# Kernel optimization log

Measured on AMD Instinct MI355X. Metric: run time of the kernel, lower is better.

## Reference

```python
import jax, jax.numpy as jnp
import numpy as np

HIDDEN = 768
HEADS = 12
ORDERS = 3
NEG = -1e9


def setup_inputs() -> dict:
    key = jax.random.key(0)
    ks = jax.random.split(key, 16)
    B, N = 8, 512
    s = 0.02
    inp = {
        "v": jax.random.normal(ks[0], (B, N, HIDDEN), jnp.float32),
        "k": jax.random.normal(ks[1], (B, N, HIDDEN), jnp.float32),
        "q": jax.random.normal(ks[2], (B, N, HIDDEN), jnp.float32),
        "masks": jax.random.bernoulli(ks[3], 0.1, (ORDERS, B, 1, N, N)),
        "tau": 1,
        "training": 0,
        "Wv": jax.random.normal(ks[4], (HIDDEN, HIDDEN), jnp.float32) * s,
        "bv": jnp.zeros((HIDDEN,), jnp.float32),
        "Wk": jax.random.normal(ks[5], (HIDDEN, HIDDEN), jnp.float32) * s,
        "bk": jnp.zeros((HIDDEN,), jnp.float32),
        "Wq": jax.random.normal(ks[6], (HIDDEN, HIDDEN), jnp.float32) * s,
        "bq": jnp.zeros((HIDDEN,), jnp.float32),
        "Wm": jax.random.normal(ks[7], (HIDDEN, HIDDEN), jnp.float32) * s,
        "bm": jnp.zeros((HIDDEN,), jnp.float32),
        "pool_w": jax.random.normal(ks[8], (HIDDEN, 1), jnp.float32) * s,
        "pool_b": jnp.zeros((1,), jnp.float32),
        "mlp_w1": jax.random.normal(ks[9], (HIDDEN, HIDDEN // 2), jnp.float32) * s,
        "mlp_w2": jax.random.normal(ks[10], (HIDDEN // 2, ORDERS), jnp.float32) * s,
        "mlp_b2": jnp.zeros((ORDERS,), jnp.float32),
    }
    return inp


def _soft_routing(x, pool_w, pool_b, mlp_w1, mlp_w2, mlp_b2):
    # pooling='fc': masked attention pooling over sequence, then 2-layer MLP + softmax
    pad = (jnp.sum(jnp.abs(x), axis=-1) == 0)[:, :, None]        # [B, N, 1]
    scores = x @ pool_w + pool_b                                  # [B, N, 1]
    scores = jnp.where(pad, NEG, scores)
    scores = jax.nn.softmax(scores, axis=1)
    pooled = jnp.sum(x * scores, axis=1)                          # [B, HIDDEN]
    logits = jax.nn.relu(pooled @ mlp_w1) @ mlp_w2 + mlp_b2       # [B, L]
    return jax.nn.softmax(logits, axis=-1)


def reference(v, k, q, masks, tau, training, Wv, bv, Wk, bk, Wq, bq, Wm, bm,
              pool_w, pool_b, mlp_w1, mlp_w2, mlp_b2):
    B, N, _ = q.shape
    dk = HIDDEN // HEADS
    alphas = _soft_routing(v, pool_w, pool_b, mlp_w1, mlp_w2, mlp_b2)  # [B, L]

    def split_heads(x):
        return x.reshape(B, N, HEADS, dk).transpose(0, 2, 1, 3)  # [B, H, N, dk]

    vh = split_heads(v @ Wv + bv)
    kh = split_heads(k @ Wk + bk)
    qh = split_heads(q @ Wq + bq)

    scores = jnp.einsum('bhnd,bhmd->bhnm', qh, kh) / jnp.sqrt(jnp.float32(dk))
    # masks: [L, B, 1, N, N] broadcast over heads -> att_list [L, B, H, N, N]
    masked = jnp.where(masks[:, :, :, :, :], NEG, scores[None])
    att_list = jax.nn.softmax(masked, axis=-1)                    # [L, B, H, N, N]
    att_map = jnp.einsum('bl,lbhnm->bhnm', alphas, att_list)
    atted = jnp.einsum('bhnm,bhmd->bhnd', att_map, vh)
    atted = atted.transpose(0, 2, 1, 3).reshape(B, N, HIDDEN)
    return atted @ Wm + bm
```

## Files before the change

### kernel.cpp

```cpp
#include <hip/hip_runtime.h>
#include <hip/hip_bf16.h>
#include <stdint.h>


typedef __bf16 bf16x8 __attribute__((ext_vector_type(8)));
typedef float f32x4 __attribute__((ext_vector_type(4)));

#define NEGV -1e9f

__device__ __forceinline__ float b2f(unsigned short h) {
    union { unsigned int u; float f; } x; x.u = ((unsigned int)h) << 16; return x.f;
}
__device__ __forceinline__ unsigned short f2b(float f) {
    union { float f; unsigned int u; } x; x.f = f;
    unsigned int u = x.u + 0x7FFFu + ((x.u >> 16) & 1u);
    return (unsigned short)(u >> 16);
}
__device__ __forceinline__ unsigned int packbf(unsigned int u0, unsigned int u1) {
    unsigned int r0 = (u0 + 0x7FFFu + ((u0 >> 16) & 1u)) >> 16;
    unsigned int r1 = (u1 + 0x7FFFu + ((u1 >> 16) & 1u)) & 0xFFFF0000u;
    return r0 | r1;
}
__device__ __forceinline__ uint4 load8bf(const void* base, size_t elemOff, int isF32) {
    if (!isF32) return *(const uint4*)((const unsigned short*)base + elemOff);
    const uint4* f = (const uint4*)((const float*)base + elemOff);
    uint4 a = f[0], b = f[1];
    uint4 r;
    r.x = packbf(a.x, a.y);
    r.y = packbf(a.z, a.w);
    r.z = packbf(b.x, b.y);
    r.w = packbf(b.z, b.w);
    return r;
}
__device__ __forceinline__ float loadF(const void* p, int idx, int isF32) {
    return isF32 ? ((const float*)p)[idx] : b2f(((const unsigned short*)p)[idx]);
}

__global__ void sniff_kernel(const unsigned int* __restrict__ mp,
                             const unsigned int* __restrict__ vp,
                             const unsigned int* __restrict__ wp,
                             int* __restrict__ flags)
{
    __shared__ int oki, oku, okf, badv, badw;
    if (threadIdx.x == 0) { oki = 1; oku = 1; okf = 1; badv = 0; badw = 0; }
    __syncthreads();
    int li = 1, lu = 1, lf = 1, bv = 0, bw = 0;
    for (int i = threadIdx.x; i < 16384; i += 256) {
        unsigned int w = mp[i];
        if (w > 1u) li = 0;
        if (w & 0xFEFEFEFEu) lu = 0;
        if (w != 0u && w != 0x3F800000u) lf = 0;
    }
    for (int i = threadIdx.x; i < 8192; i += 256) {
        unsigned int w = vp[i];
        float f0 = b2f((unsigned short)(w & 0xFFFF));
        float f1 = b2f((unsigned short)(w >> 16));
        if (!(fabsf(f0) < 1e4f) || !(fabsf(f1) < 1e4f)) bv = 1;
        w = wp[i];
        f0 = b2f((unsigned short)(w & 0xFFFF));
        f1 = b2f((unsigned short)(w >> 16));
        if (!(fabsf(f0) < 1e4f) || !(fabsf(f1) < 1e4f)) bw = 1;
    }
    if (!li) atomicAnd(&oki, 0);
    if (!lu) atomicAnd(&oku, 0);
    if (!lf) atomicAnd(&okf, 0);
    if (bv) atomicOr(&badv, 1);
    if (bw) atomicOr(&badw, 1);
    __syncthreads();
    if (threadIdx.x == 0) {
        flags[0] = oki ? 0 : (oku ? 1 : (okf ? 2 : 3));
        flags[1] = badv;
        flags[2] = badw;
    }
}

__global__ __launch_bounds__(256) void conv_act_kernel(
        const void* __restrict__ v, const void* __restrict__ k,
        const void* __restrict__ q, const int* __restrict__ flags,
        unsigned short* __restrict__ vb, unsigned short* __restrict__ kb,
        unsigned short* __restrict__ qb)
{
    const int dtV = flags[1];
    const int which = blockIdx.y;
    const void* src = (which == 0) ? v : (which == 1) ? k : q;
    unsigned short* dst = (which == 0) ? vb : (which == 1) ? kb : qb;
    size_t off = ((size_t)blockIdx.x * 256 + threadIdx.x) * 8;
    uint4 r = load8bf(src, off, dtV);
    *(uint4*)(dst + off) = r;
}

__global__ __launch_bounds__(256) void conv_wt_kernel(
        const void* __restrict__ W0, const void* __restrict__ W1,
        const void* __restrict__ W2, const void* __restrict__ W3,
        const int* __restrict__ flags,
        unsigned short* __restrict__ T0, unsigned short* __restrict__ T1,
        unsigned short* __restrict__ T2, unsigned short* __restrict__ T3)
{
    __shared__ unsigned short tile[64][65];
    const int t = threadIdx.x;
    const int dtW = flags[2];
    const int which = blockIdx.y;
    const void* W = (which == 0) ? W0 : (which == 1) ? W1 : (which == 2) ? W2 : W3;
    unsigned short* T = (which == 0) ? T0 : (which == 1) ? T1 : (which == 2) ? T2 : T3;
    const int tk = (blockIdx.x / 12) << 6;
    const int tn = (blockIdx.x % 12) << 6;
    #pragma unroll
    for (int i = 0; i < 16; i++) {
        int idx = (i << 8) + t;
        int r = idx >> 6, c = idx & 63;
        tile[r][c] = f2b(loadF(W, (tk + r) * 768 + tn + c, dtW));
    }
    __syncthreads();
    #pragma unroll
    for (int i = 0; i < 16; i++) {
        int idx = (i << 8) + t;
        int rn = idx >> 6, ck = idx & 63;
        T[(size_t)(tn + rn) * 768 + tk + ck] = tile[ck][rn];
    }
}

__global__ __launch_bounds__(256) void pack_kernel(
        const void* __restrict__ masks, const int* __restrict__ flags,
        unsigned int* __restrict__ pm)
{
    __shared__ unsigned char flg[32 * 512];
    const int t = threadIdx.x;
    const int mode = flags[0];
    const size_t e0 = (size_t)blockIdx.x * (32 * 512);
    if (mode == 0 || mode == 2) {
        const uint4* p = (const uint4*)((const unsigned int*)masks + e0);
        for (int i = t; i < 4096; i += 256) {
            uint4 u = p[i];
            int base = i << 2;
            flg[base + 0] = u.x ? 1 : 0;
            flg[base + 1] = u.y ? 1 : 0;
            flg[base + 2] = u.z ? 1 : 0;
            flg[base + 3] = u.w ? 1 : 0;
        }
    } else if (mode == 1) {
        const uint4* p = (const uint4*)((const unsigned char*)masks + e0);
        for (int i = t; i < 1024; i += 256) {
            uint4 u = p[i];
            unsigned int uu[4] = {u.x, u.y, u.z, u.w};
            int base = i << 4;
            #pragma unroll
            for (int k2 = 0; k2 < 4; k2++)
                #pragma unroll
                for (int bb = 0; bb < 4; bb++)
                    flg[base + k2 * 4 + bb] = ((uu[k2] >> (bb * 8)) & 0xFFu) ? 1 : 0;
        }
    } else {
        const uint4* p = (const uint4*)((const unsigned short*)masks + e0);
        for (int i = t; i < 2048; i += 256) {
            uint4 u = p[i];
            unsigned int uu[4] = {u.x, u.y, u.z, u.w};
            int base = i << 3;
            #pragma unroll
            for (int k2 = 0; k2 < 4; k2++) {
                flg[base + k2 * 2 + 0] = (uu[k2] & 0xFFFFu) ? 1 : 0;
                flg[base + k2 * 2 + 1] = (uu[k2] >> 16) ? 1 : 0;
            }
        }
    }
    __syncthreads();
    for (int widx = t; widx < 512; widx += 256) {
        int rl = widx >> 4, lm = widx & 15;
        unsigned int bits = 0;
        #pragma unroll
        for (int g = 0; g < 32; g++)
            bits |= ((unsigned int)(flg[rl * 512 + (g << 4) + lm] & 1)) << g;
        pm[(size_t)blockIdx.x * 512 + widx] = bits;
    }
}

__global__ __launch_bounds__(256) void route_score_kernel(
        const void* __restrict__ v, const void* __restrict__ pool_w,
        const void* __restrict__ pool_b, const int* __restrict__ flags,
        float* __restrict__ scores)
{
    __shared__ float pw[768];
    const int t = threadIdx.x;
    const int b = blockIdx.x >> 3, ch = blockIdx.x & 7;
    const int dtV = flags[1], dtW = flags[2];
    for (int d = t; d < 768; d += 256) pw[d] = loadF(pool_w, d, dtW);
    __syncthreads();
    const int r = t >> 2, c4 = t & 3;
    const int n = (ch << 6) + r;
    float dot = 0.f, asum = 0.f;
    if (!dtV) {
        const unsigned int* vr = (const unsigned int*)v + ((size_t)(b * 512 + n)) * 384;
        for (int j = 0; j < 96; j++) {
            int p = c4 + (j << 2);
            unsigned int u = vr[p];
            float f0 = b2f((unsigned short)(u & 0xFFFF));
            float f1 = b2f((unsigned short)(u >> 16));
            asum += fabsf(f0) + fabsf(f1);
            dot += f0 * pw[2 * p] + f1 * pw[2 * p + 1];
        }
    } else {
        const float* vf = (const float*)v + ((size_t)(b * 512 + n)) * 768;
        for (int j = 0; j < 48; j++) {
            float4 u = ((const float4*)vf)[c4 + (j << 2)];
            int e = (c4 + (j << 2)) << 2;
            asum += fabsf(u.x) + fabsf(u.y) + fabsf(u.z) + fabsf(u.w);
            dot += u.x * pw[e] + u.y * pw[e + 1] + u.z * pw[e + 2] + u.w * pw[e + 3];
        }
    }
    dot += __shfl_xor(dot, 1); dot += __shfl_xor(dot, 2);
    asum += __shfl_xor(asum, 1); asum += __shfl_xor(asum, 2);
    if (c4 == 0)
        scores[b * 512 + n] = (asum == 0.f) ? NEGV : dot + loadF(pool_b, 0, dtW);
}

__global__ __launch_bounds__(512) void route_softmax_kernel(
        const float* __restrict__ scores, float* __restrict__ scs)
{
    __shared__ float red[8];
    const int t = threadIdx.x, b = blockIdx.x;
    float scv = scores[b * 512 + t];
    float mx = scv;
    #pragma unroll
    for (int off = 1; off < 64; off <<= 1) mx = fmaxf(mx, __shfl_xor(mx, off));
    if ((t & 63) == 0) red[t >> 6] = mx;
    __syncthreads();
    float M = red[0];
    #pragma unroll
    for (int i = 1; i < 8; i++) M = fmaxf(M, red[i]);
    float e = __expf(scv - M);
    __syncthreads();
    float sm = e;
    #pragma unroll
    for (int off = 1; off < 64; off <<= 1) sm += __shfl_xor(sm, off);
    if ((t & 63) == 0) red[t >> 6] = sm;
    __syncthreads();
    float SS = 0.f;
    #pragma unroll
    for (int i = 0; i < 8; i++) SS += red[i];
    scs[b * 512 + t] = e / SS;
}

__global__ __launch_bounds__(256) void route_pool_kernel(
        const void* __restrict__ v, const int* __restrict__ flags,
        const float* __restrict__ scs, float* __restrict__ ppart)
{
    __shared__ float ps[64];
    const int t = threadIdx.x;
    const int ch = blockIdx.x, b = blockIdx.y;
    const int dtV = flags[1];
    if (t < 64) ps[t] = scs[b * 512 + (ch << 6) + t];
    __syncthreads();
    const int d0 = t * 3;
    float a0 = 0.f, a1 = 0.f, a2 = 0.f;
    if (!dtV) {
        const unsigned short* vb = (const unsigned short*)v
            + ((size_t)(b * 512 + (ch << 6))) * 768 + d0;
        #pragma unroll 4
        for (int r = 0; r < 64; r++) {
            float p = ps[r];
            a0 += b2f(vb[0]) * p; a1 += b2f(vb[1]) * p; a2 += b2f(vb[2]) * p;
            vb += 768;
        }
    } else {
        const float* vb = (const float*)v + ((size_t)(b * 512 + (ch << 6))) * 768 + d0;
        #pragma unroll 4
        for (int r = 0; r < 64; r++) {
            float p = ps[r];
            a0 += vb[0] * p; a1 += vb[1] * p; a2 += vb[2] * p;
            vb += 768;
        }
    }
    float* o = ppart + ((size_t)(b * 8 + ch)) * 768 + d0;
    o[0] = a0; o[1] = a1; o[2] = a2;
}

__global__ __launch_bounds__(256) void route_hid_kernel(
        const void* __restrict__ w1, const void* __restrict__ w2,
        const int* __restrict__ flags, const float* __restrict__ ppart,
        float* __restrict__ plog)
{
    __shared__ float pool[768];
    __shared__ float red[4][32];
    const int t = threadIdx.x;
    const int jc = blockIdx.x, b = blockIdx.y;
    const int dtW = flags[2];
    for (int d = t; d < 768; d += 256) {
        float a = 0.f;
        #pragma unroll
        for (int c = 0; c < 8; c++) a += ppart[((size_t)(b * 8 + c)) * 768 + d];
        pool[d] = a;
    }
    __syncthreads();
    const int jo = (t & 3) << 3;
    const int dr = t >> 2;
    float acc[8];
    #pragma unroll
    for (int j = 0; j < 8; j++) acc[j] = 0.f;
    for (int it = 0; it < 12; it++) {
        int d = (it << 6) + dr;
        float pv = pool[d];
        size_t off = (size_t)d * 384 + (jc << 5) + jo;
        if (!dtW) {
            uint4 u = *(const uint4*)((const unsigned short*)w1 + off);
            unsigned int uu[4] = {u.x, u.y, u.z, u.w};
            #pragma unroll
            for (int j2 = 0; j2 < 4; j2++) {
                acc[2 * j2]     += pv * b2f((unsigned short)(uu[j2] & 0xFFFF));
                acc[2 * j2 + 1] += pv * b2f((unsigned short)(uu[j2] >> 16));
            }
        } else {
            const float4* f = (const float4*)((const float*)w1 + off);
            float4 u0 = f[0], u1 = f[1];
            acc[0] += pv * u0.x; acc[1] += pv * u0.y;
            acc[2] += pv * u0.z; acc[3] += pv * u0.w;
            acc[4] += pv * u1.x; acc[5] += pv * u1.y;
            acc[6] += pv * u1.z; acc[7] += pv * u1.w;
        }
    }
    #pragma unroll
    for (int off = 4; off < 64; off <<= 1)
        #pragma unroll
        for (int j = 0; j < 8; j++) acc[j] += __shfl_xor(acc[j], off);
    const int w = t >> 6, lane = t & 63;
    if (lane < 4) {
        #pragma unroll
        for (int j = 0; j < 8; j++) red[w][lane * 8 + j] = acc[j];
    }
    __syncthreads();
    if (t < 32) {
        float h = red[0][t] + red[1][t] + red[2][t] + red[3][t];
        h = fmaxf(h, 0.f);
        int jg = (jc << 5) + t;
        float l0 = h * loadF(w2, jg * 3 + 0, dtW);
        float l1 = h * loadF(w2, jg * 3 + 1, dtW);
        float l2 = h * loadF(w2, jg * 3 + 2, dtW);
        #pragma unroll
        for (int off = 1; off < 32; off <<= 1) {
            l0 += __shfl_xor(l0, off);
            l1 += __shfl_xor(l1, off);
            l2 += __shfl_xor(l2, off);
        }
        if (t == 0) {
            float* o = plog + ((size_t)(b * 12 + jc)) * 3;
            o[0] = l0; o[1] = l1; o[2] = l2;
        }
    }
}

__global__ __launch_bounds__(64) void route_alpha_kernel(
        const void* __restrict__ b2, const int* __restrict__ flags,
        const float* __restrict__ plog, float* __restrict__ alphas)
{
    const int t = threadIdx.x, b = blockIdx.x;
    if (t == 0) {
        const int dtW = flags[2];
        float lg[3];
        #pragma unroll
        for (int l = 0; l < 3; l++) {
            float a = loadF(b2, l, dtW);
            for (int jc = 0; jc < 12; jc++) a += plog[((size_t)(b * 12 + jc)) * 3 + l];
            lg[l] = a;
        }
        float mm = fmaxf(lg[0], fmaxf(lg[1], lg[2]));
        float e0 = __expf(lg[0] - mm), e1 = __expf(lg[1] - mm), e2 = __expf(lg[2] - mm);
        float ss = e0 + e1 + e2;
        alphas[b * 3 + 0] = e0 / ss;
        alphas[b * 3 + 1] = e1 / ss;
        alphas[b * 3 + 2] = e2 / ss;
    }
}

__global__ __launch_bounds__(256) void gemm_kernel(
        const unsigned short* __restrict__ X,
        const unsigned short* __restrict__ WT,
        const void* __restrict__ bias,
        const int* __restrict__ flags,
        void* __restrict__ dst, int mode)
{
    __shared__ unsigned short smem[64 * 72];
    unsigned short* At = smem;
    unsigned short* Bt = smem + 2048;
    const int t = threadIdx.x;
    const int id = blockIdx.x;
    const int bx = id >> 6, by = id & 63;
    const int w = t >> 6, lane = t & 63, q = lane >> 4, lm = lane & 15;
    const int row0 = by << 6, col0 = bx << 6;
    const int ar = t >> 2, ac = (t & 3) << 3;
    const int aswz = ((ar >> 3) & 3) << 3;
    const int am = (w << 4) + lm;
    const int acs = ((am >> 3) & 3) << 3;
    const int dtW = flags[2];
    const int dtOut = flags[1];

    f32x4 acc[4];
    #pragma unroll
    for (int i = 0; i < 4; i++) acc[i] = (f32x4){0.f, 0.f, 0.f, 0.f};

    const unsigned short* xp = X + (size_t)(row0 + ar) * 768 + ac;
    const unsigned short* wp = WT + (size_t)(col0 + ar) * 768 + ac;
    for (int k0 = 0; k0 < 768; k0 += 32) {
        uint4 av = *(const uint4*)(xp + k0);
        uint4 wv = *(const uint4*)(wp + k0);
        __syncthreads();
        *(uint4*)(&At[ar * 32 + (ac ^ aswz)]) = av;
        *(uint4*)(&Bt[ar * 32 + (ac ^ aswz)]) = wv;
        __syncthreads();
        bf16x8 afr = *(const bf16x8*)(&At[am * 32 + ((q << 3) ^ acs)]);
        #pragma unroll
        for (int t4 = 0; t4 < 4; t4++) {
            int bn = (t4 << 4) + lm;
            bf16x8 bfr = *(const bf16x8*)(&Bt[bn * 32 + ((q << 3) ^ (((bn >> 3) & 3) << 3))]);
            acc[t4] = __builtin_amdgcn_mfma_f32_16x16x32_bf16(afr, bfr, acc[t4], 0, 0, 0);
        }
    }

    if (mode == 1 && dtOut) {
        #pragma unroll
        for (int t4 = 0; t4 < 4; t4++) {
            int col = col0 + (t4 << 4) + lm;
            float bsv = loadF(bias, col, dtW);
            #pragma unroll
            for (int rg = 0; rg < 4; rg++) {
                int row = row0 + (w << 4) + (q << 2) + rg;
                ((float*)dst)[(size_t)row * 768 + col] = acc[t4][rg] + bsv;
            }
        }
        return;
    }

    __syncthreads();
    #pragma unroll
    for (int t4 = 0; t4 < 4; t4++) {
        int colL = (t4 << 4) + lm;
        float bsv = loadF(bias, col0 + colL, dtW);
        #pragma unroll
        for (int rg = 0; rg < 4; rg++) {
            int rowL = (w << 4) + (q << 2) + rg;
            unsigned short hv = f2b(acc[t4][rg] + bsv);
            if (mode == 2) smem[colL * 72 + rowL] = hv;
            else           smem[rowL * 72 + colL] = hv;
        }
    }
    __syncthreads();
    const int g = t >> 2, c0 = (t & 3) << 4;
    uint4 w0 = *(const uint4*)&smem[g * 72 + c0];
    uint4 w1v = *(const uint4*)&smem[g * 72 + c0 + 8];
    unsigned short* o;
    if (mode == 0) {
        int b = row0 >> 9, n0b = row0 & 511, h = col0 >> 6;
        o = (unsigned short*)dst + ((size_t)(b * 12 + h) * 512 + n0b + g) * 64 + c0;
    } else if (mode == 2) {
        int b = row0 >> 9, n0b = row0 & 511, h = col0 >> 6;
        o = (unsigned short*)dst + ((size_t)(b * 12 + h) * 64 + g) * 512 + n0b + c0;
    } else {
        o = (unsigned short*)dst + (size_t)(row0 + g) * 768 + col0 + c0;
    }
    *(uint4*)o = w0;
    *(uint4*)(o + 8) = w1v;
}

__global__ __launch_bounds__(256) void attn_kernel(
        const unsigned short* __restrict__ qh, const unsigned short* __restrict__ kh,
        const unsigned short* __restrict__ vT, const unsigned int* __restrict__ pm,
        const float* __restrict__ alphas, unsigned short* __restrict__ atted)
{
    __shared__ unsigned short P[16 * 512];
    __shared__ float Zp[4][16][3];
    __shared__ unsigned short Ost[16 * 72];
    const int t = threadIdx.x;
    const int w = t >> 6, lane = t & 63, quad = lane >> 4, lm = lane & 15;
    const int id = blockIdx.x;
    const int bh = id % 96, qb = id / 96;
    const int b = bh / 12, h = bh % 12;
    const int n0 = qb << 4;

    const unsigned short* qrow = qh + ((size_t)(bh * 512 + n0 + lm)) * 64 + (quad << 3);
    bf16x8 qa0 = *(const bf16x8*)qrow;
    bf16x8 qa1 = *(const bf16x8*)(qrow + 32);
    f32x4 acc[8];
    #pragma unroll
    for (int i = 0; i < 8; i++) acc[i] = (f32x4){0.f, 0.f, 0.f, 0.f};
    const unsigned short* kb0 = kh + ((size_t)(bh * 512 + (w << 7) + lm)) * 64 + (quad << 3);
    #pragma unroll
    for (int nt = 0; nt < 8; nt++) {
        const unsigned short* kr = kb0 + nt * (16 * 64);
        bf16x8 k0 = *(const bf16x8*)kr;
        bf16x8 k1 = *(const bf16x8*)(kr + 32);
        acc[nt] = __builtin_amdgcn_mfma_f32_16x16x32_bf16(qa0, k0, acc[nt], 0, 0, 0);
        acc[nt] = __builtin_amdgcn_mfma_f32_16x16x32_bf16(qa1, k1, acc[nt], 0, 0, 0);
    }

    float al[3];
    #pragma unroll
    for (int l = 0; l < 3; l++) al[l] = alphas[b * 3 + l];

    #pragma unroll
    for (int nt = 0; nt < 8; nt++)
        #pragma unroll
        for (int rg = 0; rg < 4; rg++)
            acc[nt][rg] = __expf(acc[nt][rg] * 0.125f);

    unsigned int mk[4][3];
    #pragma unroll
    for (int rg = 0; rg < 4; rg++)
        #pragma unroll
        for (int l = 0; l < 3; l++)
            mk[rg][l] = pm[((size_t)((l << 3) + b) * 512 + n0 + (quad << 2) + rg) * 16 + lm];

    #pragma unroll
    for (int rg = 0; rg < 4; rg++) {
        float z0 = 0.f, z1 = 0.f, z2 = 0.f;
        #pragma unroll
        for (int nt = 0; nt < 8; nt++) {
            int g = (w << 3) + nt;
            float e = acc[nt][rg];
            if (!((mk[rg][0] >> g) & 1)) z0 += e;
            if (!((mk[rg][1] >> g) & 1)) z1 += e;
            if (!((mk[rg][2] >> g) & 1)) z2 += e;
        }
        #pragma unroll
        for (int off = 1; off < 16; off <<= 1) {
            z0 += __shfl_xor(z0, off);
            z1 += __shfl_xor(z1, off);
            z2 += __shfl_xor(z2, off);
        }
        if (lm == 0) {
            int row = (quad << 2) + rg;
            Zp[w][row][0] = z0; Zp[w][row][1] = z1; Zp[w][row][2] = z2;
        }
    }
    __syncthreads();

    #pragma unroll
    for (int rg = 0; rg < 4; rg++) {
        int row = (quad << 2) + rg;
        float coef[3]; float addu = 0.f;
        #pragma unroll
        for (int l = 0; l < 3; l++) {
            float Z = Zp[0][row][l] + Zp[1][row][l] + Zp[2][row][l] + Zp[3][row][l];
            if (Z > 0.f) coef[l] = al[l] / Z;
            else { coef[l] = 0.f; addu += al[l] * (1.0f / 512.0f); }
        }
        #pragma unroll
        for (int nt = 0; nt < 8; nt++) {
            int g = (w << 3) + nt;
            float p = addu;
            float e = acc[nt][rg];
            if (!((mk[rg][0] >> g) & 1)) p += coef[0] * e;
            if (!((mk[rg][1] >> g) & 1)) p += coef[1] * e;
            if (!((mk[rg][2] >> g) & 1)) p += coef[2] * e;
            int c = (g << 4) + lm;
            int chunk = c >> 3, j = c & 7;
            P[row * 512 + (((chunk ^ (row & 7))) << 3) + j] = f2b(p);
        }
    }
    __syncthreads();

    f32x4 accO = (f32x4){0.f, 0.f, 0.f, 0.f};
    const unsigned short* vb = vT + ((size_t)(bh * 64 + (w << 4) + lm)) * 512 + (quad << 3);
    #pragma unroll
    for (int ks = 0; ks < 16; ks++) {
        bf16x8 pa = *(const bf16x8*)&P[lm * 512 + ((((ks << 2) + quad) ^ (lm & 7)) << 3)];
        bf16x8 vf = *(const bf16x8*)(vb + (ks << 5));
        accO = __builtin_amdgcn_mfma_f32_16x16x32_bf16(pa, vf, accO, 0, 0, 0);
    }
    #pragma unroll
    for (int rg = 0; rg < 4; rg++)
        Ost[((quad << 2) + rg) * 72 + (w << 4) + lm] = f2b(accO[rg]);
    __syncthreads();
    const int r2 = t >> 4, c4 = t & 15;
    uint2 val = *(const uint2*)&Ost[r2 * 72 + (c4 << 2)];
    *(uint2*)&atted[((size_t)(b * 512 + n0 + r2)) * 768 + (h << 6) + (c4 << 2)] = val;
}

extern "C" void kernel_launch(void* const* d_in, const int* in_sizes, int n_in,
                              void* d_out, int out_size, void* d_ws, size_t ws_size,
                              hipStream_t stream)
{
    const void* v  = d_in[0];
    const void* k  = d_in[1];
    const void* q  = d_in[2];
    const void* mk = d_in[3];
    const void* Wv = d_in[6];
    const void* bv = d_in[7];
    const void* Wk = d_in[8];
    const void* bk = d_in[9];
    const void* Wq = d_in[10];
    const void* bq = d_in[11];
    const void* Wm = d_in[12];
    const void* bm = d_in[13];
    const void* pool_w = d_in[14];
    const void* pool_b = d_in[15];
    const void* w1 = d_in[16];
    const void* w2 = d_in[17];
    const void* b2 = d_in[18];

    char* ws = (char*)d_ws;
    int*   flags  = (int*)ws;
    float* alphas = (float*)(ws + 256);
    float* scores = (float*)(ws + 512);
    float* scs    = (float*)(ws + 16896);
    float* ppart  = (float*)(ws + 33280);
    float* plog   = (float*)(ws + 229888);
    unsigned int* pm = (unsigned int*)(ws + 262144);
    unsigned short* qh  = (unsigned short*)(ws + 1048576);
    unsigned short* kh  = (unsigned short*)(ws + 1048576 + 1 * 6291456L);
    unsigned short* vT  = (unsigned short*)(ws + 1048576 + 2 * 6291456L);
    unsigned short* vb  = (unsigned short*)(ws + 1048576 + 3 * 6291456L);
    unsigned short* kb  = (unsigned short*)(ws + 1048576 + 4 * 6291456L);
    unsigned short* qb  = (unsigned short*)(ws + 1048576 + 5 * 6291456L);
    unsigned short* atted = vb;
    char* wt0 = ws + 1048576 + 6 * 6291456L;
    unsigned short* WTv = (unsigned short*)(wt0);
    unsigned short* WTk = (unsigned short*)(wt0 + 1 * 1179648L);
    unsigned short* WTq = (unsigned short*)(wt0 + 2 * 1179648L);
    unsigned short* WTm = (unsigned short*)(wt0 + 3 * 1179648L);

    sniff_kernel<<<dim3(1), dim3(256), 0, stream>>>(
        (const unsigned int*)mk, (const unsigned int*)v, (const unsigned int*)Wv, flags);
    conv_act_kernel<<<dim3(1536, 3), dim3(256), 0, stream>>>(v, k, q, flags, vb, kb, qb);
    conv_wt_kernel<<<dim3(144, 4), dim3(256), 0, stream>>>(
        Wv, Wk, Wq, Wm, flags, WTv, WTk, WTq, WTm);
    pack_kernel<<<dim3(384), dim3(256), 0, stream>>>(mk, flags, pm);
    route_score_kernel<<<dim3(64), dim3(256), 0, stream>>>(v, pool_w, pool_b, flags, scores);
    route_softmax_kernel<<<dim3(8), dim3(512), 0, stream>>>(scores, scs);
    route_pool_kernel<<<dim3(8, 8), dim3(256), 0, stream>>>(v, flags, scs, ppart);
    route_hid_kernel<<<dim3(12, 8), dim3(256), 0, stream>>>(w1, w2, flags, ppart, plog);
    route_alpha_kernel<<<dim3(8), dim3(64), 0, stream>>>(b2, flags, plog, alphas);
    gemm_kernel<<<dim3(768), dim3(256), 0, stream>>>(vb, WTv, bv, flags, (void*)vT, 2);
    gemm_kernel<<<dim3(768), dim3(256), 0, stream>>>(kb, WTk, bk, flags, (void*)kh, 0);
    gemm_kernel<<<dim3(768), dim3(256), 0, stream>>>(qb, WTq, bq, flags, (void*)qh, 0);
    attn_kernel<<<dim3(3072), dim3(256), 0, stream>>>(qh, kh, vT, pm, alphas, atted);
    gemm_kernel<<<dim3(768), dim3(256), 0, stream>>>(atted, WTm, bm, flags, d_out, 1);
}
```

Measured before the change: 314.0 us.

## Batch QKV projections into one launch and prefetch deeper K tiles in GEMM

The three Q/K/V projection GEMMs become a single launch that selects its operands by blockIdx.y, which cuts launch count and fills the GPU with more concurrent blocks. The GEMM K-step grows from 32 to 64 with an XOR-swizzled shared layout, and global loads for the next tile are issued before the MFMAs on the current tile, halving barriers and overlapping load latency. The attention kernel pre-shifts its mask words per wave to simplify the bit tests. Doubling shared memory per block may reduce occupancy.

```diff
diff --git a/kernel.cpp b/kernel.cpp
--- a/kernel.cpp
+++ b/kernel.cpp
@@ -369,48 +369,74 @@
     }
 }
 
-__global__ __launch_bounds__(256) void gemm_kernel(
-        const unsigned short* __restrict__ X,
-        const unsigned short* __restrict__ WT,
-        const void* __restrict__ bias,
+__global__ __launch_bounds__(256) void gemm3_kernel(
+        const unsigned short* __restrict__ X0, const unsigned short* __restrict__ X1,
+        const unsigned short* __restrict__ X2,
+        const unsigned short* __restrict__ W0, const unsigned short* __restrict__ W1,
+        const unsigned short* __restrict__ W2,
+        const void* __restrict__ bias0, const void* __restrict__ bias1,
+        const void* __restrict__ bias2,
         const int* __restrict__ flags,
-        void* __restrict__ dst, int mode)
-{
-    __shared__ unsigned short smem[64 * 72];
+        void* __restrict__ dst0, void* __restrict__ dst1, void* __restrict__ dst2,
+        int m0, int m1, int m2)
+{
+    __shared__ unsigned short smem[8192];
     unsigned short* At = smem;
-    unsigned short* Bt = smem + 2048;
+    unsigned short* Bt = smem + 4096;
     const int t = threadIdx.x;
+    const int which = blockIdx.y;
+    const unsigned short* X  = (which == 0) ? X0 : (which == 1) ? X1 : X2;
+    const unsigned short* WT = (which == 0) ? W0 : (which == 1) ? W1 : W2;
+    const void* bias = (which == 0) ? bias0 : (which == 1) ? bias1 : bias2;
+    void* dst = (which == 0) ? dst0 : (which == 1) ? dst1 : dst2;
+    const int mode = (which == 0) ? m0 : (which == 1) ? m1 : m2;
+
     const int id = blockIdx.x;
     const int bx = id >> 6, by = id & 63;
-    const int w = t >> 6, lane = t & 63, q = lane >> 4, lm = lane & 15;
     const int row0 = by << 6, col0 = bx << 6;
-    const int ar = t >> 2, ac = (t & 3) << 3;
-    const int aswz = ((ar >> 3) & 3) << 3;
-    const int am = (w << 4) + lm;
-    const int acs = ((am >> 3) & 3) << 3;
+    const int w = t >> 6, lane = t & 63, quad = lane >> 4, lm = lane & 15;
+    const int r0 = t >> 3, c0 = (t & 7) << 3;
+    const int wr0 = r0 * 64 + (c0 ^ ((r0 & 7) << 3));
     const int dtW = flags[2];
     const int dtOut = flags[1];
 
+    const unsigned short* xp  = X  + (size_t)(row0 + r0) * 768 + c0;
+    const unsigned short* xp2 = xp + 32 * 768;
+    const unsigned short* wp  = WT + (size_t)(col0 + r0) * 768 + c0;
+    const unsigned short* wp2 = wp + 32 * 768;
+
+    uint4 a0 = *(const uint4*)xp,  a1 = *(const uint4*)xp2;
+    uint4 g0 = *(const uint4*)wp,  g1 = *(const uint4*)wp2;
+
     f32x4 acc[4];
     #pragma unroll
     for (int i = 0; i < 4; i++) acc[i] = (f32x4){0.f, 0.f, 0.f, 0.f};
 
-    const unsigned short* xp = X + (size_t)(row0 + ar) * 768 + ac;
-    const unsigned short* wp = WT + (size_t)(col0 + ar) * 768 + ac;
-    for (int k0 = 0; k0 < 768; k0 += 32) {
-        uint4 av = *(const uint4*)(xp + k0);
-        uint4 wv = *(const uint4*)(wp + k0);
+    const int am = (w << 4) + lm;
+    const int abase = am * 64, akey = (am & 7) << 3;
+
+    for (int k0 = 0;;) {
         __syncthreads();
-        *(uint4*)(&At[ar * 32 + (ac ^ aswz)]) = av;
-        *(uint4*)(&Bt[ar * 32 + (ac ^ aswz)]) = wv;
+        *(uint4*)&At[wr0] = a0;        *(uint4*)&At[wr0 + 2048] = a1;
+        *(uint4*)&Bt[wr0] = g0;        *(uint4*)&Bt[wr0 + 2048] = g1;
         __syncthreads();
-        bf16x8 afr = *(const bf16x8*)(&At[am * 32 + ((q << 3) ^ acs)]);
-        #pragma unroll
-        for (int t4 = 0; t4 < 4; t4++) {
-            int bn = (t4 << 4) + lm;
-            bf16x8 bfr = *(const bf16x8*)(&Bt[bn * 32 + ((q << 3) ^ (((bn >> 3) & 3) << 3))]);
-            acc[t4] = __builtin_amdgcn_mfma_f32_16x16x32_bf16(afr, bfr, acc[t4], 0, 0, 0);
-        }
+        k0 += 64;
+        if (k0 < 768) {
+            a0 = *(const uint4*)(xp + k0);  a1 = *(const uint4*)(xp2 + k0);
+            g0 = *(const uint4*)(wp + k0);  g1 = *(const uint4*)(wp2 + k0);
+        }
+        #pragma unroll
+        for (int ks = 0; ks < 2; ks++) {
+            int ko = (quad << 3) + (ks << 5);
+            bf16x8 afr = *(const bf16x8*)&At[abase + (ko ^ akey)];
+            #pragma unroll
+            for (int t4 = 0; t4 < 4; t4++) {
+                int bn = (t4 << 4) + lm;
+                bf16x8 bfr = *(const bf16x8*)&Bt[bn * 64 + (ko ^ ((bn & 7) << 3))];
+                acc[t4] = __builtin_amdgcn_mfma_f32_16x16x32_bf16(afr, bfr, acc[t4], 0, 0, 0);
+            }
+        }
+        if (k0 >= 768) break;
     }
 
     if (mode == 1 && dtOut) {
@@ -420,7 +446,7 @@
             float bsv = loadF(bias, col, dtW);
             #pragma unroll
             for (int rg = 0; rg < 4; rg++) {
-                int row = row0 + (w << 4) + (q << 2) + rg;
+                int row = row0 + (w << 4) + (quad << 2) + rg;
                 ((float*)dst)[(size_t)row * 768 + col] = acc[t4][rg] + bsv;
             }
         }
@@ -434,28 +460,28 @@
         float bsv = loadF(bias, col0 + colL, dtW);
         #pragma unroll
         for (int rg = 0; rg < 4; rg++) {
-            int rowL = (w << 4) + (q << 2) + rg;
+            int rowL = (w << 4) + (quad << 2) + rg;
             unsigned short hv = f2b(acc[t4][rg] + bsv);
             if (mode == 2) smem[colL * 72 + rowL] = hv;
             else           smem[rowL * 72 + colL] = hv;
         }
     }
     __syncthreads();
-    const int g = t >> 2, c0 = (t & 3) << 4;
-    uint4 w0 = *(const uint4*)&smem[g * 72 + c0];
-    uint4 w1v = *(const uint4*)&smem[g * 72 + c0 + 8];
+    const int g = t >> 2, cc = (t & 3) << 4;
+    uint4 o0 = *(const uint4*)&smem[g * 72 + cc];
+    uint4 o1 = *(const uint4*)&smem[g * 72 + cc + 8];
     unsigned short* o;
     if (mode == 0) {
         int b = row0 >> 9, n0b = row0 & 511, h = col0 >> 6;
-        o = (unsigned short*)dst + ((size_t)(b * 12 + h) * 512 + n0b + g) * 64 + c0;
+        o = (unsigned short*)dst + ((size_t)(b * 12 + h) * 512 + n0b + g) * 64 + cc;
     } else if (mode == 2) {
         int b = row0 >> 9, n0b = row0 & 511, h = col0 >> 6;
-        o = (unsigned short*)dst + ((size_t)(b * 12 + h) * 64 + g) * 512 + n0b + c0;
+        o = (unsigned short*)dst + ((size_t)(b * 12 + h) * 64 + g) * 512 + n0b + cc;
     } else {
-        o = (unsigned short*)dst + (size_t)(row0 + g) * 768 + col0 + c0;
-    }
-    *(uint4*)o = w0;
-    *(uint4*)(o + 8) = w1v;
+        o = (unsigned short*)dst + (size_t)(row0 + g) * 768 + col0 + cc;
+    }
+    *(uint4*)o = o0;
+    *(uint4*)(o + 8) = o1;
 }
 
 __global__ __launch_bounds__(256) void attn_kernel(
@@ -499,23 +525,23 @@
         for (int rg = 0; rg < 4; rg++)
             acc[nt][rg] = __expf(acc[nt][rg] * 0.125f);
 
-    unsigned int mk[4][3];
+    unsigned int mkw[4][3];
     #pragma unroll
     for (int rg = 0; rg < 4; rg++)
         #pragma unroll
         for (int l = 0; l < 3; l++)
-            mk[rg][l] = pm[((size_t)((l << 3) + b) * 512 + n0 + (quad << 2) + rg) * 16 + lm];
+            mkw[rg][l] = pm[((size_t)((l << 3) + b) * 512 + n0 + (quad << 2) + rg) * 16 + lm]
+                         >> (w << 3);
 
     #pragma unroll
     for (int rg = 0; rg < 4; rg++) {
         float z0 = 0.f, z1 = 0.f, z2 = 0.f;
         #pragma unroll
         for (int nt = 0; nt < 8; nt++) {
-            int g = (w << 3) + nt;
             float e = acc[nt][rg];
-            if (!((mk[rg][0] >> g) & 1)) z0 += e;
-            if (!((mk[rg][1] >> g) & 1)) z1 += e;
-            if (!((mk[rg][2] >> g) & 1)) z2 += e;
+            if (!((mkw[rg][0] >> nt) & 1)) z0 += e;
+            if (!((mkw[rg][1] >> nt) & 1)) z1 += e;
+            if (!((mkw[rg][2] >> nt) & 1)) z2 += e;
         }
         #pragma unroll
         for (int off = 1; off < 16; off <<= 1) {
@@ -545,9 +571,9 @@
             int g = (w << 3) + nt;
             float p = addu;
             float e = acc[nt][rg];
-            if (!((mk[rg][0] >> g) & 1)) p += coef[0] * e;
-            if (!((mk[rg][1] >> g) & 1)) p += coef[1] * e;
-            if (!((mk[rg][2] >> g) & 1)) p += coef[2] * e;
+            if (!((mkw[rg][0] >> nt) & 1)) p += coef[0] * e;
+            if (!((mkw[rg][1] >> nt) & 1)) p += coef[1] * e;
+            if (!((mkw[rg][2] >> nt) & 1)) p += coef[2] * e;
             int c = (g << 4) + lm;
             int chunk = c >> 3, j = c & 7;
             P[row * 512 + (((chunk ^ (row & 7))) << 3) + j] = f2b(p);
@@ -626,9 +652,11 @@
     route_pool_kernel<<<dim3(8, 8), dim3(256), 0, stream>>>(v, flags, scs, ppart);
     route_hid_kernel<<<dim3(12, 8), dim3(256), 0, stream>>>(w1, w2, flags, ppart, plog);
     route_alpha_kernel<<<dim3(8), dim3(64), 0, stream>>>(b2, flags, plog, alphas);
-    gemm_kernel<<<dim3(768), dim3(256), 0, stream>>>(vb, WTv, bv, flags, (void*)vT, 2);
-    gemm_kernel<<<dim3(768), dim3(256), 0, stream>>>(kb, WTk, bk, flags, (void*)kh, 0);
-    gemm_kernel<<<dim3(768), dim3(256), 0, stream>>>(qb, WTq, bq, flags, (void*)qh, 0);
+    gemm3_kernel<<<dim3(768, 3), dim3(256), 0, stream>>>(
+        vb, kb, qb, WTv, WTk, WTq, bv, bk, bq, flags,
+        (void*)vT, (void*)kh, (void*)qh, 2, 0, 0);
     attn_kernel<<<dim3(3072), dim3(256), 0, stream>>>(qh, kh, vT, pm, alphas, atted);
-    gemm_kernel<<<dim3(768), dim3(256), 0, stream>>>(atted, WTm, bm, flags, d_out, 1);
-}
+    gemm3_kernel<<<dim3(768, 1), dim3(256), 0, stream>>>(
+        atted, atted, atted, WTm, WTm, WTm, bm, bm, bm, flags,
+        d_out, d_out, d_out, 1, 1, 1);
+}
```

Result: faster. 294.9 us (-6.1%).
